# Kernel tuning notes

Measured on AMD Instinct MI355X. Metric: run time of the kernel, lower is better.

The kernel has to match this reference:

```python
import jax, jax.numpy as jnp
import numpy as np

NUM_FEATURES = 128
NUM_RADIAL = 6
NUM_ATOM_TYPES = 95
N_ATOMS = 100000
N_EDGES = 1000000


def setup_inputs() -> dict:
    key = jax.random.key(0)
    ks = jax.random.split(key, 8)
    Z = jax.random.randint(ks[0], (N_ATOMS,), 0, NUM_ATOM_TYPES, dtype=jnp.int32)
    rbf = jax.random.normal(ks[1], (N_EDGES, NUM_RADIAL), dtype=jnp.float32)
    idnb_i = jax.random.randint(ks[2], (N_EDGES,), 0, N_ATOMS, dtype=jnp.int32)
    idnb_j = jax.random.randint(ks[3], (N_EDGES,), 0, N_ATOMS, dtype=jnp.int32)
    # parameters
    s3 = np.sqrt(3.0).astype(np.float32)
    embeddings = jax.random.uniform(ks[4], (NUM_ATOM_TYPES, NUM_FEATURES), jnp.float32, -s3, s3)
    W_rbf = jax.random.normal(ks[5], (NUM_RADIAL, NUM_FEATURES), dtype=jnp.float32) * 0.3
    b_rbf = jnp.zeros((NUM_FEATURES,), jnp.float32)
    W = jax.random.normal(ks[6], (2 * NUM_FEATURES + NUM_RADIAL * 0 + 2 * NUM_FEATURES // (2 * NUM_FEATURES) * 0 + 2 * NUM_FEATURES + NUM_FEATURES - 2 * NUM_FEATURES, NUM_FEATURES), dtype=jnp.float32)  # placeholder, replaced below
    W = jax.random.normal(ks[6], (2 * NUM_FEATURES + NUM_FEATURES, NUM_FEATURES), dtype=jnp.float32) * 0.05  # (3F, F)
    b = jnp.zeros((NUM_FEATURES,), jnp.float32)
    return {"Z": Z, "rbf": rbf, "idnb_i": idnb_i, "idnb_j": idnb_j,
            "embeddings": embeddings, "W_rbf": W_rbf, "b_rbf": b_rbf, "W": W, "b": b}


def reference(Z, rbf, idnb_i, idnb_j, embeddings, W_rbf, b_rbf, W, b):
    act = jax.nn.swish
    # dense_rbf: [E, num_radial] -> [E, F]
    rbf_h = act(rbf @ W_rbf + b_rbf)
    # gather atom embeddings by atomic number, then by edge endpoints
    x = embeddings[Z]            # [N_atoms, F]
    x1 = x[idnb_i]               # [E, F]
    x2 = x[idnb_j]               # [E, F]
    h = jnp.concatenate([x1, x2, rbf_h], axis=-1)  # [E, 3F]
    return act(h @ W + b)        # [E, F]
```

## Files before the change

### kernel.cpp

```cpp
#include <hip/hip_runtime.h>
#include <hip/hip_bf16.h>
#include <stdint.h>

#define F 128
#define R 6
#define NTYPES 95
#define MTILE 128
#define HPAD 136

typedef short bf16x8 __attribute__((ext_vector_type(8)));
typedef float floatx4 __attribute__((ext_vector_type(4)));

__device__ __forceinline__ unsigned short f2bf(float x) {
    union { float f; unsigned u; } cv; cv.f = x;
    unsigned u = cv.u;
    return (unsigned short)((u + 0x7FFFu + ((u >> 16) & 1u)) >> 16);
}

__device__ __forceinline__ float swishf(float x) {
    return x * __builtin_amdgcn_rcpf(1.0f + __expf(-x));
}

__device__ __forceinline__ floatx4 swish4(floatx4 v) {
    floatx4 r;
    #pragma unroll
    for (int i = 0; i < 4; ++i) r[i] = swishf(v[i]);
    return r;
}

__global__ void prep_kernel(const float* __restrict__ emb,
                            const float* __restrict__ W,
                            const float* __restrict__ bvec,
                            float* __restrict__ embW,
                            unsigned short* __restrict__ w2t) {
    int t = threadIdx.x;
    int b = blockIdx.x;
    if (b < NTYPES) {
        int c = t >> 7, f = t & 127;
        const float* er = emb + b * F;
        const float* Wc = W + c * F * F;
        float a = 0.f;
        #pragma unroll 8
        for (int k = 0; k < F; ++k) a = __builtin_fmaf(er[k], Wc[k * F + f], a);
        embW[b * 256 + c * F + f] = a + (c == 0 ? bvec[f] : 0.f);
    } else {
        int idx = (b - NTYPES) * 256 + t;
        int n = idx >> 7, k = idx & 127;
        w2t[n * F + k] = f2bf(W[(256 + k) * F + n]);
    }
}

__global__ __launch_bounds__(256) void
edge_kernel(const int* __restrict__ Z,
            const float* __restrict__ rbf,
            const int* __restrict__ idnb_i,
            const int* __restrict__ idnb_j,
            const float* __restrict__ W_rbf,
            const float* __restrict__ b_rbf,
            const float* __restrict__ embW,
            const unsigned short* __restrict__ w2t,
            float* __restrict__ out,
            int E) {
    __shared__ __align__(16) short h_bf[MTILE * HPAD];
    __shared__ float rbf_s[MTILE * R];
    __shared__ int zi_s[MTILE];
    __shared__ int zj_s[MTILE];

    int t = threadIdx.x;
    int blk = blockIdx.x;
    long ebase = (long)blk * MTILE;

    #pragma unroll
    for (int i = 0; i < 3; ++i) {
        int idx = i * 256 + t;
        long g = ebase * R + idx;
        rbf_s[idx] = (g < (long)E * R) ? rbf[g] : 0.f;
    }
    {
        int te = t & 127;
        long e = ebase + te;
        long ec = (e < (long)E) ? e : 0;
        int zz = Z[(t < 128 ? idnb_i : idnb_j)[ec]];
        if (t < 128) zi_s[te] = zz; else zj_s[te] = zz;
    }

    int fpair = t & 63;
    int f0 = fpair * 2;
    float wr0[R], wr1[R];
    #pragma unroll
    for (int r = 0; r < R; ++r) {
        wr0[r] = W_rbf[r * F + f0];
        wr1[r] = W_rbf[r * F + f0 + 1];
    }
    float brb0 = b_rbf[f0], brb1 = b_rbf[f0 + 1];

    __syncthreads();

    int eg = t >> 6;
    for (int it = 0; it < 32; ++it) {
        int e = eg * 32 + it;
        const float2* rp2 = (const float2*)(rbf_s + e * R);
        float2 qa = rp2[0], qb = rp2[1], qc = rp2[2];
        float rv[R] = {qa.x, qa.y, qb.x, qb.y, qc.x, qc.y};
        float v0 = brb0, v1 = brb1;
        #pragma unroll
        for (int r = 0; r < R; ++r) {
            v0 = __builtin_fmaf(rv[r], wr0[r], v0);
            v1 = __builtin_fmaf(rv[r], wr1[r], v1);
        }
        v0 = swishf(v0); v1 = swishf(v1);
        unsigned packed = (unsigned)f2bf(v0) | ((unsigned)f2bf(v1) << 16);
        *(unsigned*)(&h_bf[e * HPAD + f0]) = packed;
    }

    __syncthreads();

    int w = t >> 6;
    int lid = t & 63;
    int quad = lid >> 4;
    int l15 = lid & 15;
    int wbase = w * 32;

    floatx4 acc[2][8];
    #pragma unroll
    for (int et = 0; et < 2; ++et)
        #pragma unroll
        for (int ft = 0; ft < 8; ++ft)
            acc[et][ft] = (floatx4){0.f, 0.f, 0.f, 0.f};

    const bf16x8* w2v = (const bf16x8*)w2t;
    #pragma unroll
    for (int ks = 0; ks < 4; ++ks) {
        bf16x8 b0 = *(const bf16x8*)(&h_bf[(wbase + l15) * HPAD + ks * 32 + quad * 8]);
        bf16x8 b1 = *(const bf16x8*)(&h_bf[(wbase + 16 + l15) * HPAD + ks * 32 + quad * 8]);
        #pragma unroll
        for (int ft = 0; ft < 8; ++ft) {
            bf16x8 afr = w2v[(ft * 16 + l15) * 16 + ks * 4 + quad];
            acc[0][ft] = __builtin_amdgcn_mfma_f32_16x16x32_bf16(afr, b0, acc[0][ft], 0, 0, 0);
            acc[1][ft] = __builtin_amdgcn_mfma_f32_16x16x32_bf16(afr, b1, acc[1][ft], 0, 0, 0);
        }
    }

    #pragma unroll
    for (int et = 0; et < 2; ++et) {
        int e_loc = wbase + et * 16 + l15;
        long e_g = ebase + e_loc;
        bool ok = e_g < (long)E;
        int zi = zi_s[e_loc], zj = zj_s[e_loc];
        const floatx4* p0 = (const floatx4*)(embW + zi * 256);
        const floatx4* p1 = (const floatx4*)(embW + zj * 256 + F);
        float* op = out + e_g * F;
        #pragma unroll
        for (int ft = 0; ft < 8; ++ft) {
            int f4 = ft * 4 + quad;
            floatx4 v = acc[et][ft] + p0[f4] + p1[f4];
            floatx4 r = swish4(v);
            if (ok) *(floatx4*)(op + f4 * 4) = r;
        }
    }
}

extern "C" void kernel_launch(void* const* d_in, const int* in_sizes, int n_in,
                              void* d_out, int out_size, void* d_ws, size_t ws_size,
                              hipStream_t stream) {
    const int*   Z     = (const int*)d_in[0];
    const float* rbf   = (const float*)d_in[1];
    const int*   id_i  = (const int*)d_in[2];
    const int*   id_j  = (const int*)d_in[3];
    const float* emb   = (const float*)d_in[4];
    const float* W_rbf = (const float*)d_in[5];
    const float* b_rbf = (const float*)d_in[6];
    const float* W     = (const float*)d_in[7];
    const float* bvec  = (const float*)d_in[8];
    float* out = (float*)d_out;
    int E = in_sizes[2];

    float* embW = (float*)d_ws;
    unsigned short* w2t = (unsigned short*)((char*)d_ws + 97280);

    prep_kernel<<<NTYPES + 64, 256, 0, stream>>>(emb, W, bvec, embW, w2t);
    int grid = (E + MTILE - 1) / MTILE;
    edge_kernel<<<grid, 256, 0, stream>>>(Z, rbf, id_i, id_j, W_rbf, b_rbf,
                                          embW, w2t, out, E);
}
```

Measured before the change: 768.4 us.

## Compute rbf features in registers directly as MFMA B fragments, drop LDS staging

Removes the shared-memory staging of rbf, atom types and the bf16 hidden tile. Each lane now loads its own edge's rbf values and atom types and builds its MFMA B fragment in registers from a repacked W_rbf/bias table written by the prep kernel. The tile shrinks to 64 edges (16 per wave) and launch bounds target 4 blocks per CU, which removes both __syncthreads barriers and raises occupancy. The cost is that rbf_h is recomputed redundantly across the four quads per lane group, and each lane issues more scattered global loads.

```diff
diff --git a/kernel.cpp b/kernel.cpp
--- a/kernel.cpp
+++ b/kernel.cpp
@@ -5,8 +5,7 @@
 #define F 128
 #define R 6
 #define NTYPES 95
-#define MTILE 128
-#define HPAD 136
+#define MTILE 64
 
 typedef short bf16x8 __attribute__((ext_vector_type(8)));
 typedef float floatx4 __attribute__((ext_vector_type(4)));
@@ -31,8 +30,11 @@
 __global__ void prep_kernel(const float* __restrict__ emb,
                             const float* __restrict__ W,
                             const float* __restrict__ bvec,
+                            const float* __restrict__ W_rbf,
+                            const float* __restrict__ b_rbf,
                             float* __restrict__ embW,
-                            unsigned short* __restrict__ w2t) {
+                            unsigned short* __restrict__ w2t,
+                            float* __restrict__ wrtp) {
     int t = threadIdx.x;
     int b = blockIdx.x;
     if (b < NTYPES) {
@@ -43,120 +45,85 @@
         #pragma unroll 8
         for (int k = 0; k < F; ++k) a = __builtin_fmaf(er[k], Wc[k * F + f], a);
         embW[b * 256 + c * F + f] = a + (c == 0 ? bvec[f] : 0.f);
-    } else {
+    } else if (b < NTYPES + 64) {
         int idx = (b - NTYPES) * 256 + t;
         int n = idx >> 7, k = idx & 127;
         w2t[n * F + k] = f2bf(W[(256 + k) * F + n]);
+    } else {
+        int idx = (b - NTYPES - 64) * 256 + t;
+        int f = idx >> 3, r = idx & 7;
+        float v = (r < R) ? W_rbf[r * F + f] : (r == R ? b_rbf[f] : 0.f);
+        wrtp[idx] = v;
     }
 }
 
-__global__ __launch_bounds__(256) void
+__global__ __launch_bounds__(256, 4) void
 edge_kernel(const int* __restrict__ Z,
             const float* __restrict__ rbf,
             const int* __restrict__ idnb_i,
             const int* __restrict__ idnb_j,
-            const float* __restrict__ W_rbf,
-            const float* __restrict__ b_rbf,
             const float* __restrict__ embW,
             const unsigned short* __restrict__ w2t,
+            const float* __restrict__ wrtp,
             float* __restrict__ out,
             int E) {
-    __shared__ __align__(16) short h_bf[MTILE * HPAD];
-    __shared__ float rbf_s[MTILE * R];
-    __shared__ int zi_s[MTILE];
-    __shared__ int zj_s[MTILE];
-
     int t = threadIdx.x;
-    int blk = blockIdx.x;
-    long ebase = (long)blk * MTILE;
-
-    #pragma unroll
-    for (int i = 0; i < 3; ++i) {
-        int idx = i * 256 + t;
-        long g = ebase * R + idx;
-        rbf_s[idx] = (g < (long)E * R) ? rbf[g] : 0.f;
-    }
-    {
-        int te = t & 127;
-        long e = ebase + te;
-        long ec = (e < (long)E) ? e : 0;
-        int zz = Z[(t < 128 ? idnb_i : idnb_j)[ec]];
-        if (t < 128) zi_s[te] = zz; else zj_s[te] = zz;
-    }
-
-    int fpair = t & 63;
-    int f0 = fpair * 2;
-    float wr0[R], wr1[R];
-    #pragma unroll
-    for (int r = 0; r < R; ++r) {
-        wr0[r] = W_rbf[r * F + f0];
-        wr1[r] = W_rbf[r * F + f0 + 1];
-    }
-    float brb0 = b_rbf[f0], brb1 = b_rbf[f0 + 1];
-
-    __syncthreads();
-
-    int eg = t >> 6;
-    for (int it = 0; it < 32; ++it) {
-        int e = eg * 32 + it;
-        const float2* rp2 = (const float2*)(rbf_s + e * R);
-        float2 qa = rp2[0], qb = rp2[1], qc = rp2[2];
-        float rv[R] = {qa.x, qa.y, qb.x, qb.y, qc.x, qc.y};
-        float v0 = brb0, v1 = brb1;
-        #pragma unroll
-        for (int r = 0; r < R; ++r) {
-            v0 = __builtin_fmaf(rv[r], wr0[r], v0);
-            v1 = __builtin_fmaf(rv[r], wr1[r], v1);
-        }
-        v0 = swishf(v0); v1 = swishf(v1);
-        unsigned packed = (unsigned)f2bf(v0) | ((unsigned)f2bf(v1) << 16);
-        *(unsigned*)(&h_bf[e * HPAD + f0]) = packed;
-    }
-
-    __syncthreads();
-
     int w = t >> 6;
     int lid = t & 63;
     int quad = lid >> 4;
     int l15 = lid & 15;
-    int wbase = w * 32;
 
-    floatx4 acc[2][8];
+    long e = (long)blockIdx.x * MTILE + w * 16 + l15;
+    bool ok = e < (long)E;
+    long ec = ok ? e : (long)(E - 1);
+
+    int zi = Z[idnb_i[ec]];
+    int zj = Z[idnb_j[ec]];
+    const float2* rp = (const float2*)(rbf + ec * R);
+    float2 r01 = rp[0], r23 = rp[1], r45 = rp[2];
+
+    floatx4 acc[8];
     #pragma unroll
-    for (int et = 0; et < 2; ++et)
-        #pragma unroll
-        for (int ft = 0; ft < 8; ++ft)
-            acc[et][ft] = (floatx4){0.f, 0.f, 0.f, 0.f};
+    for (int ft = 0; ft < 8; ++ft) acc[ft] = (floatx4){0.f, 0.f, 0.f, 0.f};
 
     const bf16x8* w2v = (const bf16x8*)w2t;
+    const floatx4* wp = (const floatx4*)wrtp;
+
     #pragma unroll
     for (int ks = 0; ks < 4; ++ks) {
-        bf16x8 b0 = *(const bf16x8*)(&h_bf[(wbase + l15) * HPAD + ks * 32 + quad * 8]);
-        bf16x8 b1 = *(const bf16x8*)(&h_bf[(wbase + 16 + l15) * HPAD + ks * 32 + quad * 8]);
+        int fb = ks * 32 + quad * 8;
+        union { unsigned short s[8]; bf16x8 v; } bu;
+        #pragma unroll
+        for (int j = 0; j < 8; ++j) {
+            int f = fb + j;
+            floatx4 wa = wp[f * 2];
+            floatx4 wb = wp[f * 2 + 1];
+            float v = wb[2];
+            v = __builtin_fmaf(r01.x, wa[0], v);
+            v = __builtin_fmaf(r01.y, wa[1], v);
+            v = __builtin_fmaf(r23.x, wa[2], v);
+            v = __builtin_fmaf(r23.y, wa[3], v);
+            v = __builtin_fmaf(r45.x, wb[0], v);
+            v = __builtin_fmaf(r45.y, wb[1], v);
+            bu.s[j] = f2bf(swishf(v));
+        }
+        bf16x8 bfr = bu.v;
         #pragma unroll
         for (int ft = 0; ft < 8; ++ft) {
             bf16x8 afr = w2v[(ft * 16 + l15) * 16 + ks * 4 + quad];
-            acc[0][ft] = __builtin_amdgcn_mfma_f32_16x16x32_bf16(afr, b0, acc[0][ft], 0, 0, 0);
-            acc[1][ft] = __builtin_amdgcn_mfma_f32_16x16x32_bf16(afr, b1, acc[1][ft], 0, 0, 0);
+            acc[ft] = __builtin_amdgcn_mfma_f32_16x16x32_bf16(afr, bfr, acc[ft], 0, 0, 0);
         }
     }
 
+    const floatx4* p0 = (const floatx4*)(embW + zi * 256);
+    const floatx4* p1 = (const floatx4*)(embW + zj * 256 + F);
+    float* op = out + e * F;
     #pragma unroll
-    for (int et = 0; et < 2; ++et) {
-        int e_loc = wbase + et * 16 + l15;
-        long e_g = ebase + e_loc;
-        bool ok = e_g < (long)E;
-        int zi = zi_s[e_loc], zj = zj_s[e_loc];
-        const floatx4* p0 = (const floatx4*)(embW + zi * 256);
-        const floatx4* p1 = (const floatx4*)(embW + zj * 256 + F);
-        float* op = out + e_g * F;
-        #pragma unroll
-        for (int ft = 0; ft < 8; ++ft) {
-            int f4 = ft * 4 + quad;
-            floatx4 v = acc[et][ft] + p0[f4] + p1[f4];
-            floatx4 r = swish4(v);
-            if (ok) *(floatx4*)(op + f4 * 4) = r;
-        }
+    for (int ft = 0; ft < 8; ++ft) {
+        int f4 = ft * 4 + quad;
+        floatx4 v = acc[ft] + p0[f4] + p1[f4];
+        floatx4 r = swish4(v);
+        if (ok) *(floatx4*)(op + f4 * 4) = r;
     }
 }
 
@@ -177,9 +144,11 @@
 
     float* embW = (float*)d_ws;
     unsigned short* w2t = (unsigned short*)((char*)d_ws + 97280);
+    float* wrtp = (float*)((char*)d_ws + 97280 + 32768);
 
-    prep_kernel<<<NTYPES + 64, 256, 0, stream>>>(emb, W, bvec, embW, w2t);
+    prep_kernel<<<NTYPES + 64 + 4, 256, 0, stream>>>(emb, W, bvec, W_rbf, b_rbf,
+                                                     embW, w2t, wrtp);
     int grid = (E + MTILE - 1) / MTILE;
-    edge_kernel<<<grid, 256, 0, stream>>>(Z, rbf, id_i, id_j, W_rbf, b_rbf,
-                                          embW, w2t, out, E);
+    edge_kernel<<<grid, 256, 0, stream>>>(Z, rbf, id_i, id_j,
+                                          embW, w2t, wrtp, out, E);
 }
```

After: 924.5 us. 20.3% more time.
